# Kernel tuning notes

Measured on AMD Instinct MI355X. Metric: run time of the kernel, lower is better.

The kernel has to match this reference:

```python
import jax, jax.numpy as jnp
import numpy as np

B, N, E, H = 4, 1024, 1024, 16
D = E // H  # head dim = 64
SCALE = float(E) ** 0.5  # NOTE: original scales by embedding_dim**0.5, not head_dim


def setup_inputs() -> dict:
    key = jax.random.key(0)
    ks = jax.random.split(key, 9)
    sd = 1.0 / np.sqrt(E)
    return {
        "q": jax.random.normal(ks[0], (B, N, E), jnp.float32),
        "k": jax.random.normal(ks[1], (B, N, E), jnp.float32),
        "v": jax.random.normal(ks[2], (B, N, E), jnp.float32),
        "Wq": jax.random.normal(ks[3], (E, E), jnp.float32) * sd,
        "bq": jax.random.normal(ks[4], (E,), jnp.float32) * sd,
        "Wk": jax.random.normal(ks[5], (E, E), jnp.float32) * sd,
        "bk": jax.random.normal(ks[6], (E,), jnp.float32) * sd,
        "Wv": jax.random.normal(ks[7], (E, E), jnp.float32) * sd,
        "bv": jax.random.normal(ks[8], (E,), jnp.float32) * sd,
    }


def _split_heads(x):
    # (b, n, h*d) -> (b, h, n, d)
    b, n, _ = x.shape
    return x.reshape(b, n, H, D).transpose(0, 2, 1, 3)


def reference(q, k, v, Wq, bq, Wk, bk, Wv, bv):
    q = _split_heads(q @ Wq.T + bq)
    k = _split_heads(k @ Wk.T + bk)
    v = _split_heads(v @ Wv.T + bv)
    # full NxN scores, scaled by embedding_dim**0.5 (as in original)
    attn = jnp.einsum('bhnd,bhld->bhnl', q, k) / SCALE
    attn = jax.nn.softmax(attn, axis=-1)
    # dropout omitted (eval mode)
    # faithful to original non-standard einsum: sums attn over l, broadcasts v
    out = jnp.einsum('bhnl,bhnd->bhnd', attn, v)
    return (out, attn)
```

## Files before the change

### kernel.cpp

```cpp
#include <hip/hip_runtime.h>
#include <hip/hip_bf16.h>
#include <math.h>

#define Bc 4
#define Nc 1024
#define Ec 1024
#define Hc 16
#define Dc 64
#define Mc 4096
#define OUT0_ELEMS 4194304
#define ATTN_ELEMS 67108864ULL
#define SCRATCH_OFF 58720256
#define NTK 32

typedef __attribute__((ext_vector_type(4))) float f32x4;
typedef __attribute__((ext_vector_type(16))) float f32x16;
typedef __attribute__((ext_vector_type(8))) short s16x8;

__device__ __forceinline__ short f2bf(float f) {
    union { __bf16 h; short s; } c; c.h = (__bf16)f; return c.s;
}

typedef const __attribute__((address_space(1))) char gch;
typedef __attribute__((address_space(3))) char lch;
__device__ __forceinline__ void gload16(const short* g, short* l) {
    __builtin_amdgcn_global_load_lds((gch*)g, (lch*)l, 16, 0, 0);
}

__global__ __launch_bounds__(256)
void cvt_kernel(const float* __restrict__ xq, const float* __restrict__ xk,
                const float* __restrict__ wq, const float* __restrict__ wk,
                short* __restrict__ dst)
{
    const int which = blockIdx.y;
    const float* src; size_t n, off;
    switch (which) {
      case 0:  src = xq; n = 4194304; off = 0;       break;
      case 1:  src = xk; n = 4194304; off = 4194304; break;
      case 2:  src = wq; n = 1048576; off = 8388608; break;
      default: src = wk; n = 1048576; off = 9437184; break;
    }
    const size_t i = ((size_t)blockIdx.x * 256 + threadIdx.x) * 8;
    if (i >= n) return;
    f32x4 a = *(const f32x4*)(src + i);
    f32x4 b = *(const f32x4*)(src + i + 4);
    s16x8 o;
    o[0] = f2bf(a[0]); o[1] = f2bf(a[1]); o[2] = f2bf(a[2]); o[3] = f2bf(a[3]);
    o[4] = f2bf(b[0]); o[5] = f2bf(b[1]); o[6] = f2bf(b[2]); o[7] = f2bf(b[3]);
    *(s16x8*)(dst + off + i) = o;
}

__global__ __launch_bounds__(256)
void proj_kernel(const short* __restrict__ xall, const short* __restrict__ wall,
                 const float* __restrict__ bq, const float* __restrict__ bk,
                 short* __restrict__ qws, short* __restrict__ kws)
{
    const int sel = blockIdx.z;
    const short* X = xall + (size_t)sel * 4194304;
    const short* W = wall + (size_t)sel * 1048576;
    const float* bias = (sel == 0) ? bq : bk;

    __shared__ __align__(16) short lA[3][128 * 32];
    __shared__ __align__(16) short lB[3][128 * 32];

    const int t    = threadIdx.x;
    const int lane = t & 63;
    const int w    = t >> 6;
    const int wr   = w >> 1, wc = w & 1;
    const int li   = lane & 15, g = lane >> 4;
    const int bm   = blockIdx.x * 128;
    const int bn   = blockIdx.y * 128;

    const int sr = lane >> 2;
    const int c_ = lane & 3;

    f32x4 acc[4][4];
#pragma unroll
    for (int i = 0; i < 4; ++i)
#pragma unroll
        for (int j = 0; j < 4; ++j)
            acc[i][j] = (f32x4){0.f, 0.f, 0.f, 0.f};

#define STAGE(buf, kt)                                                        \
    {                                                                         \
        const int kb = (kt) * 32;                                             \
        _Pragma("unroll")                                                     \
        for (int j = 0; j < 2; ++j) {                                         \
            const int row = w * 32 + j * 16 + sr;                             \
            const int cg  = (c_ ^ ((row >> 1) & 3)) * 8;                      \
            gload16(X + (size_t)(bm + row) * Ec + kb + cg,                    \
                    &lA[buf][(w * 32 + j * 16) * 32]);                        \
            gload16(W + (size_t)(bn + row) * Ec + kb + cg,                    \
                    &lB[buf][(w * 32 + j * 16) * 32]);                        \
        }                                                                     \
    }

    STAGE(0, 0);
    STAGE(1, 1);
    asm volatile("s_waitcnt vmcnt(4)" ::: "memory");
    __builtin_amdgcn_s_barrier();

    for (int kt = 0; kt < NTK; ++kt) {
        const int cur = kt % 3;
        if (kt + 2 < NTK) STAGE((kt + 2) % 3, kt + 2);

        s16x8 aF[4], bF[4];
#pragma unroll
        for (int mt = 0; mt < 4; ++mt) {
            const int r = wr * 64 + mt * 16 + li;
            aF[mt] = *(const s16x8*)&lA[cur][r * 32 + ((g ^ ((r >> 1) & 3)) * 8)];
        }
#pragma unroll
        for (int nt = 0; nt < 4; ++nt) {
            const int r = wc * 64 + nt * 16 + li;
            bF[nt] = *(const s16x8*)&lB[cur][r * 32 + ((g ^ ((r >> 1) & 3)) * 8)];
        }
#pragma unroll
        for (int mt = 0; mt < 4; ++mt)
#pragma unroll
            for (int nt = 0; nt < 4; ++nt)
                acc[mt][nt] = __builtin_amdgcn_mfma_f32_16x16x32_bf16(
                    aF[mt], bF[nt], acc[mt][nt], 0, 0, 0);

        if (kt + 2 < NTK) {
            asm volatile("s_waitcnt vmcnt(4)" ::: "memory");
        } else {
            asm volatile("s_waitcnt vmcnt(0)" ::: "memory");
        }
        __builtin_amdgcn_s_barrier();
    }
#undef STAGE

    short* dstBF = (sel == 0) ? qws : kws;
#pragma unroll
    for (int nt = 0; nt < 4; ++nt) {
        const int col = bn + wc * 64 + nt * 16 + li;
        const float bcol = bias[col];
        const int h = col >> 6, d = col & 63;
#pragma unroll
        for (int mt = 0; mt < 4; ++mt) {
#pragma unroll
            for (int r = 0; r < 4; ++r) {
                const int row = bm + wr * 64 + mt * 16 + g * 4 + r;
                const int bb = row >> 10, n = row & 1023;
                const size_t off = ((size_t)(bb * Hc + h) * Nc + n) * Dc + d;
                dstBF[off] = f2bf(acc[mt][nt][r] + bcol);
            }
        }
    }
}

__global__ __launch_bounds__(512, 4)
void fused_kernel(const short* __restrict__ qws, const short* __restrict__ kws,
                  float* __restrict__ attnOut,
                  const float* __restrict__ vin, const float* __restrict__ Wv,
                  const float* __restrict__ bv, float* __restrict__ out0)
{
    __shared__ __align__(16) char smemRaw[37888];

    const int bid = blockIdx.x;
    const int t   = threadIdx.x;
    const int lane = t & 63;

    if (bid < 256) {
        short (*lsA)[128 * 32] = (short (*)[128 * 32])(smemRaw);
        short (*lsB)[128 * 32] = (short (*)[128 * 32])(smemRaw + 16384);

        const int bm = (bid & 31) * 128;
        const int bn = (bid >> 5) * 128;
        const int w  = t >> 6;
        const int wr = w >> 2;
        const int wc = w & 3;
        const int li = lane & 15, g = lane >> 4;

        const int r0 = t >> 2;
        const int c2 = t & 3;
        const float* Xs = vin + (size_t)(bm + r0) * Ec + c2 * 8;
        const float* Ws = Wv  + (size_t)(bn + r0) * Ec + c2 * 8;
        const int aoff = r0 * 32 + ((c2 ^ ((r0 >> 1) & 3)) * 8);

        f32x4 acc[4][2];
#pragma unroll
        for (int i = 0; i < 4; ++i)
#pragma unroll
            for (int j = 0; j < 2; ++j)
                acc[i][j] = (f32x4){0.f, 0.f, 0.f, 0.f};

        f32x4 eA0, eA1, eB0, eB1;
        f32x4 oA0, oA1, oB0, oB1;

#define VLOAD(a0, a1, b0, b1, kt)                                             \
        {                                                                     \
            const float* pa = Xs + (kt) * 32;                                 \
            const float* pb = Ws + (kt) * 32;                                 \
            a0 = *(const f32x4*)(pa); a1 = *(const f32x4*)(pa + 4);           \
            b0 = *(const f32x4*)(pb); b1 = *(const f32x4*)(pb + 4);           \
        }

#define VWRITE(buf, a0, a1, b0, b1)                                           \
        {                                                                     \
            s16x8 ha, hb;                                                     \
            _Pragma("unroll")                                                 \
            for (int i = 0; i < 4; ++i) {                                     \
                ha[i] = f2bf(a0[i]); ha[i + 4] = f2bf(a1[i]);                 \
                hb[i] = f2bf(b0[i]); hb[i + 4] = f2bf(b1[i]);                 \
            }                                                                 \
            *(s16x8*)&lsA[buf][aoff] = ha;                                    \
            *(s16x8*)&lsB[buf][aoff] = hb;                                    \
        }

#define VCOMPUTE(buf)                                                         \
        {                                                                     \
            s16x8 aF[4], bF[2];                                               \
            _Pragma("unroll")                                                 \
            for (int mt = 0; mt < 4; ++mt) {                                  \
                const int r = wr * 64 + mt * 16 + li;                         \
                aF[mt] = *(const s16x8*)&lsA[buf][r * 32 + ((g ^ ((r >> 1) & 3)) * 8)]; \
            }                                                                 \
            _Pragma("unroll")                                                 \
            for (int nt = 0; nt < 2; ++nt) {                                  \
                const int r = wc * 32 + nt * 16 + li;                         \
                bF[nt] = *(const s16x8*)&lsB[buf][r * 32 + ((g ^ ((r >> 1) & 3)) * 8)]; \
            }                                                                 \
            _Pragma("unroll")                                                 \
            for (int mt = 0; mt < 4; ++mt)                                    \
                _Pragma("unroll")                                             \
                for (int nt = 0; nt < 2; ++nt)                                \
                    acc[mt][nt] = __builtin_amdgcn_mfma_f32_16x16x32_bf16(    \
                        aF[mt], bF[nt], acc[mt][nt], 0, 0, 0);                \
        }

        VLOAD(eA0, eA1, eB0, eB1, 0);
        VLOAD(oA0, oA1, oB0, oB1, 1);
        VWRITE(0, eA0, eA1, eB0, eB1);
        VLOAD(eA0, eA1, eB0, eB1, 2);
        asm volatile("s_waitcnt lgkmcnt(0)" ::: "memory");
        __builtin_amdgcn_s_barrier();

        for (int tt = 0; tt < NTK; tt += 2) {
            VCOMPUTE(0);
            if (tt + 1 < NTK) {
                VWRITE(1, oA0, oA1, oB0, oB1);
                if (tt + 3 < NTK) VLOAD(oA0, oA1, oB0, oB1, tt + 3);
            }
            asm volatile("s_waitcnt lgkmcnt(0)" ::: "memory");
            __builtin_amdgcn_s_barrier();

            if (tt + 1 < NTK) {
                VCOMPUTE(1);
                if (tt + 2 < NTK) {
                    VWRITE(0, eA0, eA1, eB0, eB1);
                    if (tt + 4 < NTK) VLOAD(eA0, eA1, eB0, eB1, tt + 4);
                }
                asm volatile("s_waitcnt lgkmcnt(0)" ::: "memory");
                __builtin_amdgcn_s_barrier();
            }
        }
#undef VCOMPUTE
#undef VWRITE
#undef VLOAD

#pragma unroll
        for (int nt = 0; nt < 2; ++nt) {
            const int col = bn + wc * 32 + nt * 16 + li;
            const float bcol = bv[col];
            const int h = col >> 6, d = col & 63;
#pragma unroll
            for (int mt = 0; mt < 4; ++mt) {
#pragma unroll
                for (int r = 0; r < 4; ++r) {
                    const int row = bm + wr * 64 + mt * 16 + g * 4 + r;
                    const int bb = row >> 10, n = row & 1023;
                    out0[((size_t)(bb * Hc + h) * Nc + n) * Dc + d] =
                        acc[mt][nt][r] + bcol;
                }
            }
        }
        return;
    }

    short* lsK = (short*)smemRaw;
    short* lsQ = (short*)(smemRaw + 32768);
    float (*red)[32] = (float (*)[32])(smemRaw + 36864);

    const int abid = bid - 256;
    const int rb  = (abid >> 3) & 31;
    const int bh  = ((abid & 7) << 3) | (abid >> 8);
    const int w  = t >> 6;
    const int li = lane & 31;
    const int hi = lane >> 5;

    const short* Qb = qws + (size_t)bh * (Nc * Dc);
    const short* Kb = kws + (size_t)bh * (Nc * Dc);

    const int gcs = ((lane & 7) ^ (lane >> 3)) * 8;
    const int gr8 = lane >> 3;

    if (w < 4)
        gload16(Qb + (size_t)(rb * 32 + w * 8 + gr8) * Dc + gcs,
                &lsQ[(w * 8) * Dc]);

#define STAGEK(tile)                                                          \
    {                                                                         \
        _Pragma("unroll")                                                     \
        for (int j = 0; j < 4; ++j) {                                         \
            const int rb8 = w * 32 + j * 8;                                   \
            gload16(Kb + (size_t)((tile) * 256 + rb8 + gr8) * Dc + gcs,       \
                    &lsK[rb8 * Dc]);                                          \
        }                                                                     \
    }

    STAGEK(0);
    __syncthreads();

    s16x8 qF[4];
#pragma unroll
    for (int s = 0; s < 4; ++s) {
        const int slot = (hi + 2 * s) ^ (li & 7);
        qF[s] = *(const s16x8*)&lsQ[li * Dc + slot * 8];
    }

    f32x16 acc[4];
#pragma unroll
    for (int i = 0; i < 4; ++i) acc[i] = (f32x16)(0.f);

#pragma unroll
    for (int tile = 0; tile < 4; ++tile) {
        const int lr = w * 32 + li;
#pragma unroll
        for (int s = 0; s < 4; ++s) {
            const int slot = (hi + 2 * s) ^ (li & 7);
            s16x8 kf = *(const s16x8*)&lsK[lr * Dc + slot * 8];
            acc[tile] = __builtin_amdgcn_mfma_f32_32x32x16_bf16(
                qF[s], kf, acc[tile], 0, 0, 0);
        }
        __syncthreads();
        if (tile < 3) {
            STAGEK(tile + 1);
            __syncthreads();
        }
    }
#undef STAGEK

    const float c = 1.44269504f / 32.0f;
    float sm[16];
#pragma unroll
    for (int r = 0; r < 16; ++r) sm[r] = 0.f;
#pragma unroll
    for (int ct = 0; ct < 4; ++ct) {
#pragma unroll
        for (int r = 0; r < 16; ++r) {
            float p = __builtin_amdgcn_exp2f(acc[ct][r] * c);
            acc[ct][r] = p;
            sm[r] += p;
        }
    }
#pragma unroll
    for (int r = 0; r < 16; ++r) {
#pragma unroll
        for (int off = 1; off < 32; off <<= 1)
            sm[r] += __shfl_xor(sm[r], off);
    }

    if (li == 0) {
#pragma unroll
        for (int r = 0; r < 16; ++r)
            red[w][(r & 3) + 8 * (r >> 2) + 4 * hi] = sm[r];
    }
    __syncthreads();
#pragma unroll
    for (int r = 0; r < 16; ++r) {
        const int row = (r & 3) + 8 * (r >> 2) + 4 * hi;
        float s = red[0][row] + red[1][row] + red[2][row] + red[3][row] +
                  red[4][row] + red[5][row] + red[6][row] + red[7][row];
        sm[r] = 1.0f / s;
    }

    float* outp = attnOut + (size_t)bh * (Nc * Nc) + (size_t)(rb * 32) * Nc;
#pragma unroll
    for (int ct = 0; ct < 4; ++ct) {
        const int col = ct * 256 + w * 32 + li;
#pragma unroll
        for (int r = 0; r < 16; ++r) {
            const int row = (r & 3) + 8 * (r >> 2) + 4 * hi;
            __builtin_nontemporal_store(acc[ct][r] * sm[r],
                                        &outp[(size_t)row * Nc + col]);
        }
    }
}

extern "C" void kernel_launch(void* const* d_in, const int* in_sizes, int n_in,
                              void* d_out, int out_size, void* d_ws, size_t ws_size,
                              hipStream_t stream) {
    const float* q  = (const float*)d_in[0];
    const float* k  = (const float*)d_in[1];
    const float* v  = (const float*)d_in[2];
    const float* Wq = (const float*)d_in[3];
    const float* bq = (const float*)d_in[4];
    const float* Wk = (const float*)d_in[5];
    const float* bk = (const float*)d_in[6];
    const float* Wv = (const float*)d_in[7];
    const float* bv = (const float*)d_in[8];

    float* out0 = (float*)d_out;
    float* attn = (float*)d_out + OUT0_ELEMS;

    short* s16  = (short*)(attn + SCRATCH_OFF);
    short* xall = s16;
    short* wall = s16 + 8388608;

    short* qws = (short*)d_ws;
    short* kws = qws + (size_t)Mc * Ec;

    cvt_kernel<<<dim3(2048, 4), 256, 0, stream>>>(q, k, Wq, Wk, s16);
    proj_kernel<<<dim3(32, 8, 2), 256, 0, stream>>>(
        xall, wall, bq, bk, qws, kws);
    fused_kernel<<<2304, 512, 0, stream>>>(qws, kws, attn, v, Wv, bv, out0);
}
```

Before: 115.5 us.

## Split pipeline into batched mega-kernel launches overlapping projection, conversion and attention

```diff
diff --git a/kernel.cpp b/kernel.cpp
--- a/kernel.cpp
+++ b/kernel.cpp
@@ -9,7 +9,6 @@
 #define Dc 64
 #define Mc 4096
 #define OUT0_ELEMS 4194304
-#define ATTN_ELEMS 67108864ULL
 #define SCRATCH_OFF 58720256
 #define NTK 32
 
@@ -28,133 +27,35 @@
 }
 
 __global__ __launch_bounds__(256)
-void cvt_kernel(const float* __restrict__ xq, const float* __restrict__ xk,
-                const float* __restrict__ wq, const float* __restrict__ wk,
-                short* __restrict__ dst)
+void cvt0_kernel(const float* __restrict__ wq, const float* __restrict__ wk,
+                 const float* __restrict__ xq, const float* __restrict__ xk,
+                 short* __restrict__ xall, short* __restrict__ wall)
 {
-    const int which = blockIdx.y;
-    const float* src; size_t n, off;
-    switch (which) {
-      case 0:  src = xq; n = 4194304; off = 0;       break;
-      case 1:  src = xk; n = 4194304; off = 4194304; break;
-      case 2:  src = wq; n = 1048576; off = 8388608; break;
-      default: src = wk; n = 1048576; off = 9437184; break;
-    }
-    const size_t i = ((size_t)blockIdx.x * 256 + threadIdx.x) * 8;
-    if (i >= n) return;
+    const int b = blockIdx.x;
+    const float* src; short* dst; size_t ofs;
+    if (b < 512)       { src = wq; dst = wall;           ofs = (size_t)b * 2048; }
+    else if (b < 1024) { src = wk; dst = wall + 1048576; ofs = (size_t)(b - 512) * 2048; }
+    else if (b < 2048) { src = xq; dst = xall;           ofs = (size_t)(b - 1024) * 2048; }
+    else               { src = xk; dst = xall + 4194304; ofs = (size_t)(b - 2048) * 2048; }
+    const size_t i = ofs + (size_t)threadIdx.x * 8;
     f32x4 a = *(const f32x4*)(src + i);
-    f32x4 b = *(const f32x4*)(src + i + 4);
+    f32x4 c = *(const f32x4*)(src + i + 4);
     s16x8 o;
     o[0] = f2bf(a[0]); o[1] = f2bf(a[1]); o[2] = f2bf(a[2]); o[3] = f2bf(a[3]);
-    o[4] = f2bf(b[0]); o[5] = f2bf(b[1]); o[6] = f2bf(b[2]); o[7] = f2bf(b[3]);
-    *(s16x8*)(dst + off + i) = o;
+    o[4] = f2bf(c[0]); o[5] = f2bf(c[1]); o[6] = f2bf(c[2]); o[7] = f2bf(c[3]);
+    *(s16x8*)(dst + i) = o;
 }
 
-__global__ __launch_bounds__(256)
-void proj_kernel(const short* __restrict__ xall, const short* __restrict__ wall,
+__global__ __launch_bounds__(512, 4)
+void mega_kernel(int nV, int nP, int pBase, int nA, int aBase,
+                 const short* __restrict__ qws_r, const short* __restrict__ kws_r,
+                 short* __restrict__ qws, short* __restrict__ kws,
+                 float* __restrict__ attnOut,
+                 const float* __restrict__ vin, const float* __restrict__ Wv,
+                 const float* __restrict__ bv, float* __restrict__ out0,
+                 const short* __restrict__ xall, const short* __restrict__ wall,
                  const float* __restrict__ bq, const float* __restrict__ bk,
-                 short* __restrict__ qws, short* __restrict__ kws)
-{
-    const int sel = blockIdx.z;
-    const short* X = xall + (size_t)sel * 4194304;
-    const short* W = wall + (size_t)sel * 1048576;
-    const float* bias = (sel == 0) ? bq : bk;
-
-    __shared__ __align__(16) short lA[3][128 * 32];
-    __shared__ __align__(16) short lB[3][128 * 32];
-
-    const int t    = threadIdx.x;
-    const int lane = t & 63;
-    const int w    = t >> 6;
-    const int wr   = w >> 1, wc = w & 1;
-    const int li   = lane & 15, g = lane >> 4;
-    const int bm   = blockIdx.x * 128;
-    const int bn   = blockIdx.y * 128;
-
-    const int sr = lane >> 2;
-    const int c_ = lane & 3;
-
-    f32x4 acc[4][4];
-#pragma unroll
-    for (int i = 0; i < 4; ++i)
-#pragma unroll
-        for (int j = 0; j < 4; ++j)
-            acc[i][j] = (f32x4){0.f, 0.f, 0.f, 0.f};
-
-#define STAGE(buf, kt)                                                        \
-    {                                                                         \
-        const int kb = (kt) * 32;                                             \
-        _Pragma("unroll")                                                     \
-        for (int j = 0; j < 2; ++j) {                                         \
-            const int row = w * 32 + j * 16 + sr;                             \
-            const int cg  = (c_ ^ ((row >> 1) & 3)) * 8;                      \
-            gload16(X + (size_t)(bm + row) * Ec + kb + cg,                    \
-                    &lA[buf][(w * 32 + j * 16) * 32]);                        \
-            gload16(W + (size_t)(bn + row) * Ec + kb + cg,                    \
-                    &lB[buf][(w * 32 + j * 16) * 32]);                        \
-        }                                                                     \
-    }
-
-    STAGE(0, 0);
-    STAGE(1, 1);
-    asm volatile("s_waitcnt vmcnt(4)" ::: "memory");
-    __builtin_amdgcn_s_barrier();
-
-    for (int kt = 0; kt < NTK; ++kt) {
-        const int cur = kt % 3;
-        if (kt + 2 < NTK) STAGE((kt + 2) % 3, kt + 2);
-
-        s16x8 aF[4], bF[4];
-#pragma unroll
-        for (int mt = 0; mt < 4; ++mt) {
-            const int r = wr * 64 + mt * 16 + li;
-            aF[mt] = *(const s16x8*)&lA[cur][r * 32 + ((g ^ ((r >> 1) & 3)) * 8)];
-        }
-#pragma unroll
-        for (int nt = 0; nt < 4; ++nt) {
-            const int r = wc * 64 + nt * 16 + li;
-            bF[nt] = *(const s16x8*)&lB[cur][r * 32 + ((g ^ ((r >> 1) & 3)) * 8)];
-        }
-#pragma unroll
-        for (int mt = 0; mt < 4; ++mt)
-#pragma unroll
-            for (int nt = 0; nt < 4; ++nt)
-                acc[mt][nt] = __builtin_amdgcn_mfma_f32_16x16x32_bf16(
-                    aF[mt], bF[nt], acc[mt][nt], 0, 0, 0);
-
-        if (kt + 2 < NTK) {
-            asm volatile("s_waitcnt vmcnt(4)" ::: "memory");
-        } else {
-            asm volatile("s_waitcnt vmcnt(0)" ::: "memory");
-        }
-        __builtin_amdgcn_s_barrier();
-    }
-#undef STAGE
-
-    short* dstBF = (sel == 0) ? qws : kws;
-#pragma unroll
-    for (int nt = 0; nt < 4; ++nt) {
-        const int col = bn + wc * 64 + nt * 16 + li;
-        const float bcol = bias[col];
-        const int h = col >> 6, d = col & 63;
-#pragma unroll
-        for (int mt = 0; mt < 4; ++mt) {
-#pragma unroll
-            for (int r = 0; r < 4; ++r) {
-                const int row = bm + wr * 64 + mt * 16 + g * 4 + r;
-                const int bb = row >> 10, n = row & 1023;
-                const size_t off = ((size_t)(bb * Hc + h) * Nc + n) * Dc + d;
-                dstBF[off] = f2bf(acc[mt][nt][r] + bcol);
-            }
-        }
-    }
-}
-
-__global__ __launch_bounds__(512, 4)
-void fused_kernel(const short* __restrict__ qws, const short* __restrict__ kws,
-                  float* __restrict__ attnOut,
-                  const float* __restrict__ vin, const float* __restrict__ Wv,
-                  const float* __restrict__ bv, float* __restrict__ out0)
+                 const float* __restrict__ xqf, const float* __restrict__ xkf)
 {
     __shared__ __align__(16) char smemRaw[37888];
 
@@ -162,12 +63,12 @@
     const int t   = threadIdx.x;
     const int lane = t & 63;
 
-    if (bid < 256) {
+    if (bid < nV) {
         short (*lsA)[128 * 32] = (short (*)[128 * 32])(smemRaw);
         short (*lsB)[128 * 32] = (short (*)[128 * 32])(smemRaw + 16384);
-
-        const int bm = (bid & 31) * 128;
-        const int bn = (bid >> 5) * 128;
+        const int vb = bid;
+        const int bm = (vb & 31) * 128;
+        const int bn = (vb >> 5) * 128;
         const int w  = t >> 6;
         const int wr = w >> 2;
         const int wc = w & 3;
@@ -279,113 +180,225 @@
         return;
     }
 
-    short* lsK = (short*)smemRaw;
-    short* lsQ = (short*)(smemRaw + 32768);
-    float (*red)[32] = (float (*)[32])(smemRaw + 36864);
-
-    const int abid = bid - 256;
-    const int rb  = (abid >> 3) & 31;
-    const int bh  = ((abid & 7) << 3) | (abid >> 8);
-    const int w  = t >> 6;
-    const int li = lane & 31;
-    const int hi = lane >> 5;
-
-    const short* Qb = qws + (size_t)bh * (Nc * Dc);
-    const short* Kb = kws + (size_t)bh * (Nc * Dc);
-
-    const int gcs = ((lane & 7) ^ (lane >> 3)) * 8;
-    const int gr8 = lane >> 3;
-
-    if (w < 4)
-        gload16(Qb + (size_t)(rb * 32 + w * 8 + gr8) * Dc + gcs,
-                &lsQ[(w * 8) * Dc]);
+    if (bid < nV + nP) {
+        short (*lpA)[128 * 32] = (short (*)[128 * 32])(smemRaw);
+        short (*lpB)[128 * 32] = (short (*)[128 * 32])(smemRaw + 16384);
+
+        const int pb  = bid - nV;
+        const int sel = pb >> 7;
+        const int r7  = pb & 127;
+        const int bx  = pBase + (r7 >> 3);
+        const int by  = r7 & 7;
+        const short* X = xall + (size_t)sel * 4194304;
+        const short* W = wall + (size_t)sel * 1048576;
+        const float* bias = sel ? bk : bq;
+        short* dst = sel ? kws : qws;
+
+        const int bm = bx * 128;
+        const int bn = by * 128;
+        const int w  = t >> 6;
+        const int wr = w >> 2;
+        const int wcn = w & 3;
+        const int li = lane & 15, g = lane >> 4;
+
+        const int srow = w * 16 + (lane >> 2);
+        const int c_   = lane & 3;
+        const int cg   = (c_ ^ ((srow >> 1) & 3)) * 8;
+
+        f32x4 acc[4][2];
+#pragma unroll
+        for (int i = 0; i < 4; ++i)
+#pragma unroll
+            for (int j = 0; j < 2; ++j)
+                acc[i][j] = (f32x4){0.f, 0.f, 0.f, 0.f};
+
+#define PSTAGE(buf, kt)                                                       \
+        {                                                                     \
+            gload16(X + (size_t)(bm + srow) * Ec + (kt) * 32 + cg,            \
+                    &lpA[buf][(w * 16) * 32]);                                \
+            gload16(W + (size_t)(bn + srow) * Ec + (kt) * 32 + cg,            \
+                    &lpB[buf][(w * 16) * 32]);                                \
+        }
+
+        PSTAGE(0, 0);
+        PSTAGE(1, 1);
+
+        for (int kt = 0; kt < NTK; ++kt) {
+            const int cur = kt & 1;
+            if (kt < NTK - 1) {
+                asm volatile("s_waitcnt vmcnt(2)" ::: "memory");
+            } else {
+                asm volatile("s_waitcnt vmcnt(0)" ::: "memory");
+            }
+            __builtin_amdgcn_s_barrier();
+
+            s16x8 aF[4], bF[2];
+#pragma unroll
+            for (int mt = 0; mt < 4; ++mt) {
+                const int r = wr * 64 + mt * 16 + li;
+                aF[mt] = *(const s16x8*)&lpA[cur][r * 32 + ((g ^ ((r >> 1) & 3)) * 8)];
+            }
+#pragma unroll
+            for (int nt = 0; nt < 2; ++nt) {
+                const int r = wcn * 32 + nt * 16 + li;
+                bF[nt] = *(const s16x8*)&lpB[cur][r * 32 + ((g ^ ((r >> 1) & 3)) * 8)];
+            }
+#pragma unroll
+            for (int mt = 0; mt < 4; ++mt)
+#pragma unroll
+                for (int nt = 0; nt < 2; ++nt)
+                    acc[mt][nt] = __builtin_amdgcn_mfma_f32_16x16x32_bf16(
+                        aF[mt], bF[nt], acc[mt][nt], 0, 0, 0);
+
+            asm volatile("s_waitcnt lgkmcnt(0)" ::: "memory");
+            __builtin_amdgcn_s_barrier();
+            if (kt + 2 < NTK) PSTAGE(cur, kt + 2);
+        }
+#undef PSTAGE
+
+#pragma unroll
+        for (int nt = 0; nt < 2; ++nt) {
+            const int col = bn + wcn * 32 + nt * 16 + li;
+            const float bcol = bias[col];
+            const int h = col >> 6, d = col & 63;
+#pragma unroll
+            for (int mt = 0; mt < 4; ++mt) {
+#pragma unroll
+                for (int r = 0; r < 4; ++r) {
+                    const int row = bm + wr * 64 + mt * 16 + g * 4 + r;
+                    const int bb = row >> 10, n = row & 1023;
+                    dst[((size_t)(bb * Hc + h) * Nc + n) * Dc + d] =
+                        f2bf(acc[mt][nt][r] + bcol);
+                }
+            }
+        }
+        return;
+    }
+
+    if (bid < nV + nP + nA) {
+        short* lsK = (short*)smemRaw;
+        short* lsQ = (short*)(smemRaw + 32768);
+        float (*red)[32] = (float (*)[32])(smemRaw + 36864);
+
+        const int abid = bid - nV - nP;
+        const int rb  = (abid >> 3) & 31;
+        const int bh  = aBase + (((abid & 7) << 2) | (abid >> 8));
+        const int w  = t >> 6;
+        const int li = lane & 31;
+        const int hi = lane >> 5;
+
+        const short* Qb = qws_r + (size_t)bh * (Nc * Dc);
+        const short* Kb = kws_r + (size_t)bh * (Nc * Dc);
+
+        const int gcs = ((lane & 7) ^ (lane >> 3)) * 8;
+        const int gr8 = lane >> 3;
+
+        if (w < 4)
+            gload16(Qb + (size_t)(rb * 32 + w * 8 + gr8) * Dc + gcs,
+                    &lsQ[(w * 8) * Dc]);
 
 #define STAGEK(tile)                                                          \
-    {                                                                         \
-        _Pragma("unroll")                                                     \
-        for (int j = 0; j < 4; ++j) {                                         \
-            const int rb8 = w * 32 + j * 8;                                   \
-            gload16(Kb + (size_t)((tile) * 256 + rb8 + gr8) * Dc + gcs,       \
-                    &lsK[rb8 * Dc]);                                          \
-        }                                                                     \
-    }
-
-    STAGEK(0);
-    __syncthreads();
-
-    s16x8 qF[4];
-#pragma unroll
-    for (int s = 0; s < 4; ++s) {
-        const int slot = (hi + 2 * s) ^ (li & 7);
-        qF[s] = *(const s16x8*)&lsQ[li * Dc + slot * 8];
-    }
-
-    f32x16 acc[4];
-#pragma unroll
-    for (int i = 0; i < 4; ++i) acc[i] = (f32x16)(0.f);
-
-#pragma unroll
-    for (int tile = 0; tile < 4; ++tile) {
-        const int lr = w * 32 + li;
+        {                                                                     \
+            _Pragma("unroll")                                                 \
+            for (int j = 0; j < 4; ++j) {                                     \
+                const int rb8 = w * 32 + j * 8;                               \
+                gload16(Kb + (size_t)((tile) * 256 + rb8 + gr8) * Dc + gcs,   \
+                        &lsK[rb8 * Dc]);                                      \
+            }                                                                 \
+        }
+
+        STAGEK(0);
+        __syncthreads();
+
+        s16x8 qF[4];
 #pragma unroll
         for (int s = 0; s < 4; ++s) {
             const int slot = (hi + 2 * s) ^ (li & 7);
-            s16x8 kf = *(const s16x8*)&lsK[lr * Dc + slot * 8];
-            acc[tile] = __builtin_amdgcn_mfma_f32_32x32x16_bf16(
-                qF[s], kf, acc[tile], 0, 0, 0);
+            qF[s] = *(const s16x8*)&lsQ[li * Dc + slot * 8];
+        }
+
+        f32x16 acc[4];
+#pragma unroll
+        for (int i = 0; i < 4; ++i) acc[i] = (f32x16)(0.f);
+
+#pragma unroll
+        for (int tile = 0; tile < 4; ++tile) {
+            const int lr = w * 32 + li;
+#pragma unroll
+            for (int s = 0; s < 4; ++s) {
+                const int slot = (hi + 2 * s) ^ (li & 7);
+                s16x8 kf = *(const s16x8*)&lsK[lr * Dc + slot * 8];
+                acc[tile] = __builtin_amdgcn_mfma_f32_32x32x16_bf16(
+                    qF[s], kf, acc[tile], 0, 0, 0);
+            }
+            __syncthreads();
+            if (tile < 3) {
+                STAGEK(tile + 1);
+                __syncthreads();
+            }
+        }
+#undef STAGEK
+
+        const float c = 1.44269504f / 32.0f;
+        float sm[16];
+#pragma unroll
+        for (int r = 0; r < 16; ++r) sm[r] = 0.f;
+#pragma unroll
+        for (int ct = 0; ct < 4; ++ct) {
+#pragma unroll
+            for (int r = 0; r < 16; ++r) {
+                float p = __builtin_amdgcn_exp2f(acc[ct][r] * c);
+                acc[ct][r] = p;
+                sm[r] += p;
+            }
+        }
+#pragma unroll
+        for (int r = 0; r < 16; ++r) {
+#pragma unroll
+            for (int off = 1; off < 32; off <<= 1)
+                sm[r] += __shfl_xor(sm[r], off);
+        }
+
+        if (li == 0) {
+#pragma unroll
+            for (int r = 0; r < 16; ++r)
+                red[w][(r & 3) + 8 * (r >> 2) + 4 * hi] = sm[r];
         }
         __syncthreads();
-        if (tile < 3) {
-            STAGEK(tile + 1);
-            __syncthreads();
-        }
-    }
-#undef STAGEK
-
-    const float c = 1.44269504f / 32.0f;
-    float sm[16];
-#pragma unroll
-    for (int r = 0; r < 16; ++r) sm[r] = 0.f;
-#pragma unroll
-    for (int ct = 0; ct < 4; ++ct) {
-#pragma unroll
-        for (int r = 0; r < 16; ++r) {
-            float p = __builtin_amdgcn_exp2f(acc[ct][r] * c);
-            acc[ct][r] = p;
-            sm[r] += p;
-        }
-    }
-#pragma unroll
-    for (int r = 0; r < 16; ++r) {
-#pragma unroll
-        for (int off = 1; off < 32; off <<= 1)
-            sm[r] += __shfl_xor(sm[r], off);
-    }
-
-    if (li == 0) {
-#pragma unroll
-        for (int r = 0; r < 16; ++r)
-            red[w][(r & 3) + 8 * (r >> 2) + 4 * hi] = sm[r];
-    }
-    __syncthreads();
-#pragma unroll
-    for (int r = 0; r < 16; ++r) {
-        const int row = (r & 3) + 8 * (r >> 2) + 4 * hi;
-        float s = red[0][row] + red[1][row] + red[2][row] + red[3][row] +
-                  red[4][row] + red[5][row] + red[6][row] + red[7][row];
-        sm[r] = 1.0f / s;
-    }
-
-    float* outp = attnOut + (size_t)bh * (Nc * Nc) + (size_t)(rb * 32) * Nc;
-#pragma unroll
-    for (int ct = 0; ct < 4; ++ct) {
-        const int col = ct * 256 + w * 32 + li;
 #pragma unroll
         for (int r = 0; r < 16; ++r) {
             const int row = (r & 3) + 8 * (r >> 2) + 4 * hi;
-            __builtin_nontemporal_store(acc[ct][r] * sm[r],
-                                        &outp[(size_t)row * Nc + col]);
-        }
+            float s = red[0][row] + red[1][row] + red[2][row] + red[3][row] +
+                      red[4][row] + red[5][row] + red[6][row] + red[7][row];
+            sm[r] = 1.0f / s;
+        }
+
+        float* outp = attnOut + (size_t)bh * (Nc * Nc) + (size_t)(rb * 32) * Nc;
+#pragma unroll
+        for (int ct = 0; ct < 4; ++ct) {
+            const int col = ct * 256 + w * 32 + li;
+#pragma unroll
+            for (int r = 0; r < 16; ++r) {
+                const int row = (r & 3) + 8 * (r >> 2) + 4 * hi;
+                __builtin_nontemporal_store(acc[ct][r] * sm[r],
+                                            &outp[(size_t)row * Nc + col]);
+            }
+        }
+        return;
+    }
+
+    {
+        const int cb = bid - nV - nP - nA;
+        const int seg = (cb >> 9);
+        const float* src = seg ? xkf : xqf;
+        short* dstx = (short*)(xall + (seg ? 4194304 : 0));
+        const size_t i = 2097152 + (size_t)(cb & 511) * 4096 + (size_t)t * 8;
+        f32x4 a = *(const f32x4*)(src + i);
+        f32x4 c2 = *(const f32x4*)(src + i + 4);
+        s16x8 o;
+        o[0] = f2bf(a[0]); o[1] = f2bf(a[1]); o[2] = f2bf(a[2]); o[3] = f2bf(a[3]);
+        o[4] = f2bf(c2[0]); o[5] = f2bf(c2[1]); o[6] = f2bf(c2[2]); o[7] = f2bf(c2[3]);
+        *(s16x8*)(dstx + i) = o;
     }
 }
 
@@ -412,8 +425,17 @@
     short* qws = (short*)d_ws;
     short* kws = qws + (size_t)Mc * Ec;
 
-    cvt_kernel<<<dim3(2048, 4), 256, 0, stream>>>(q, k, Wq, Wk, s16);
-    proj_kernel<<<dim3(32, 8, 2), 256, 0, stream>>>(
-        xall, wall, bq, bk, qws, kws);
-    fused_kernel<<<2304, 512, 0, stream>>>(qws, kws, attn, v, Wv, bv, out0);
+    cvt0_kernel<<<3072, 256, 0, stream>>>(Wq, Wk, q, k, xall, wall);
+    mega_kernel<<<1536, 512, 0, stream>>>(
+        256, 256, 0, 0, 0,
+        qws, kws, qws, kws, attn, v, Wv, bv, out0,
+        xall, wall, bq, bk, q, k);
+    mega_kernel<<<1280, 512, 0, stream>>>(
+        0, 256, 16, 1024, 0,
+        qws, kws, qws, kws, attn, v, Wv, bv, out0,
+        xall, wall, bq, bk, q, k);
+    mega_kernel<<<1024, 512, 0, stream>>>(
+        0, 0, 0, 1024, 32,
+        qws, kws, qws, kws, attn, v, Wv, bv, out0,
+        xall, wall, bq, bk, q, k);
 }
```

New measurement: 124.6 us. 7.9% more time.
